# Optimization experiments

Hardware: AMD Instinct MI355X
Metric: run time of the kernel (lower is better)

The kernel has to match this reference:

```python
import jax, jax.numpy as jnp
import numpy as np

HIDDEN = 5120
N_HEADS = 16           # 128 total heads / DEVICE_NUM=8
Q_LORA = 1536
KV_LORA = 512
NOPE = 128
ROPE = 64
QK_DIM = NOPE + ROPE   # 192
V_DIM = 128
EPS = 1e-6
ROPE_BASE = 10000.0
SCALE_BY_DEVICE = 1.0 / 8.0
SOFTMAX_SCALE = QK_DIM ** -0.5
B, S = 1, 2048


def rms_norm(x, w, eps=EPS):
    v = jnp.mean(jnp.square(x), axis=-1, keepdims=True)
    return x * jax.lax.rsqrt(v + eps) * w


def rotate_half(x):
    h = x.shape[-1] // 2
    return jnp.concatenate([-x[..., h:], x[..., :h]], axis=-1)


def interleave(x):
    # DeepSeek rope layout: view(b,h,s,d//2,2).transpose(-1,-2).reshape(b,h,s,d)
    b, h, s, d = x.shape
    return jnp.swapaxes(x.reshape(b, h, s, d // 2, 2), -1, -2).reshape(b, h, s, d)


def setup_inputs() -> dict:
    key = jax.random.key(0)
    ks = jax.random.split(key, 8)
    w = 0.02
    hidden_states = jax.random.normal(ks[0], (B, S, HIDDEN), dtype=jnp.float32)
    position_ids = jnp.arange(S, dtype=jnp.int64 if jax.config.jax_enable_x64 else jnp.int32)[None, :]
    causal = jnp.tril(jnp.ones((S, S), dtype=bool))
    attention_mask = jnp.where(causal, 0.0, -1e9).astype(jnp.float32)[None, None]
    return {
        'hidden_states': hidden_states,
        'position_ids': position_ids,
        'attention_mask': attention_mask,
        'ln_w': jnp.ones((HIDDEN,), jnp.float32),
        'wq_a': jax.random.normal(ks[1], (Q_LORA, HIDDEN), jnp.float32) * w,
        'q_a_ln_w': jnp.ones((Q_LORA,), jnp.float32),
        'wq_b': jax.random.normal(ks[2], (N_HEADS * QK_DIM, Q_LORA), jnp.float32) * w,
        'wkv_a': jax.random.normal(ks[3], (KV_LORA + ROPE, HIDDEN), jnp.float32) * w,
        'kv_a_ln_w': jnp.ones((KV_LORA,), jnp.float32),
        'wkv_b': jax.random.normal(ks[4], (N_HEADS * (NOPE + V_DIM), KV_LORA), jnp.float32) * w,
        'wo': jax.random.normal(ks[5], (HIDDEN, N_HEADS * V_DIM), jnp.float32) * w,
    }


def reference(hidden_states, position_ids, attention_mask, ln_w, wq_a, q_a_ln_w,
              wq_b, wkv_a, kv_a_ln_w, wkv_b, wo):
    b, s, _ = hidden_states.shape
    residual = hidden_states * SCALE_BY_DEVICE
    h = rms_norm(hidden_states, ln_w)

    # Q low-rank decompression: q_a_proj -> RMSNorm -> q_b_proj
    q = rms_norm(h @ wq_a.T, q_a_ln_w) @ wq_b.T
    q = q.reshape(b, s, N_HEADS, QK_DIM).transpose(0, 2, 1, 3)  # b,h,s,192
    q_nope, q_pe = q[..., :NOPE], q[..., NOPE:]

    # KV low-rank: kv_a_proj_with_mqa -> split -> RMSNorm -> kv_b_proj
    ckv = h @ wkv_a.T                                           # b,s,512+64
    c_kv, k_pe = ckv[..., :KV_LORA], ckv[..., KV_LORA:]
    k_pe = k_pe[:, None, :, :]                                  # b,1,s,64
    kv = rms_norm(c_kv, kv_a_ln_w) @ wkv_b.T
    kv = kv.reshape(b, s, N_HEADS, NOPE + V_DIM).transpose(0, 2, 1, 3)
    k_nope, v = kv[..., :NOPE], kv[..., NOPE:]

    # RoPE (DeepSeek interleaved layout)
    inv_freq = 1.0 / (ROPE_BASE ** (jnp.arange(0, ROPE, 2, dtype=jnp.float32) / ROPE))
    freqs = position_ids.astype(jnp.float32)[..., None] * inv_freq  # b,s,32
    emb = jnp.concatenate([freqs, freqs], axis=-1)                  # b,s,64
    cos = jnp.cos(emb)[:, None]                                     # b,1,s,64
    sin = jnp.sin(emb)[:, None]
    q_pe = interleave(q_pe)
    k_pe = interleave(k_pe)
    q_pe = q_pe * cos + rotate_half(q_pe) * sin
    k_pe = k_pe * cos + rotate_half(k_pe) * sin

    k = jnp.concatenate([k_nope, jnp.broadcast_to(k_pe, (b, N_HEADS, s, ROPE))], axis=-1)
    qf = jnp.concatenate([q_nope, q_pe], axis=-1)

    scores = jnp.einsum('bhqd,bhkd->bhqk', qf, k) * SOFTMAX_SCALE + attention_mask
    attn = jax.nn.softmax(scores.astype(jnp.float32), axis=-1).astype(qf.dtype)
    out = jnp.einsum('bhqk,bhkd->bhqd', attn, v)                    # b,h,s,128
    out = out.transpose(0, 2, 1, 3).reshape(b, s, N_HEADS * V_DIM) @ wo.T

    hidden_states = residual + out
    return (hidden_states.astype(jnp.float32), k.astype(jnp.float32), v.astype(jnp.float32))
```

## Files before the change

kernel.cpp:

```cpp
#include <hip/hip_runtime.h>
#include <hip/hip_bf16.h>

typedef __hip_bfloat16 bf16;
typedef __attribute__((ext_vector_type(8))) short bf16x8;
typedef __attribute__((ext_vector_type(4))) float f32x4;

#define S_LEN   2048
#define HIDDEN  5120
#define NHEADS  16
#define QLORA   1536
#define KVLORA  512
#define QKD     192
#define VD      128
#define QN      (NHEADS*QKD)
#define KVN     (NHEADS*(128+VD))
#define QCKN    2112
#define SM_SCALE 0.07216878364870322f

__device__ __forceinline__ f32x4 mfma16(bf16x8 a, bf16x8 b, f32x4 c) {
  return __builtin_amdgcn_mfma_f32_16x16x32_bf16(a, b, c, 0, 0, 0);
}
__device__ __forceinline__ void g2l16(const void* g, void* l) {
  __builtin_amdgcn_global_load_lds((const __attribute__((address_space(1))) void*)g,
                                   (__attribute__((address_space(3))) void*)l, 16, 0, 0);
}
__device__ __forceinline__ bf16x8 ld8(const bf16* p) { return *(const bf16x8*)p; }

__global__ void init_k(float4* __restrict__ qa_ckv, int n_qa,
                       float4* __restrict__ q_f, int n_q)
{
  int i = blockIdx.x * 256 + threadIdx.x;
  if (i < n_qa) { qa_ckv[i] = (float4){0.f, 0.f, 0.f, 0.f}; return; }
  if ((i -= n_qa) < n_q) q_f[i] = (float4){0.f, 0.f, 0.f, 0.f};
}

__global__ void cvt_multi(const float* s0, bf16* d0, int n0,
                          const float* s1, bf16* d1, int n1,
                          const float* s2, bf16* d2, int n2,
                          const float* s3, bf16* d3, int n3,
                          const float* s4, bf16* d4, int n4s)
{
  int i = blockIdx.x * 256 + threadIdx.x;
  const float* s; bf16* d;
  if (i < n0) { s = s0; d = d0; }
  else if ((i -= n0) < n1) { s = s1; d = d1; }
  else if ((i -= n1) < n2) { s = s2; d = d2; }
  else if ((i -= n2) < n3) { s = s3; d = d3; }
  else if ((i -= n3) < n4s) { s = s4; d = d4; }
  else return;
  const float4 v = ((const float4*)s)[i];
  union { bf16 b[4]; unsigned long long u; } pk;
  pk.b[0] = __float2bfloat16(v.x);
  pk.b[1] = __float2bfloat16(v.y);
  pk.b[2] = __float2bfloat16(v.z);
  pk.b[3] = __float2bfloat16(v.w);
  *(unsigned long long*)(d + (size_t)i * 4) = pk.u;
}

__global__ void rmsnorm_k(const float* __restrict__ in, int istride, int C,
                          const float* __restrict__ w,
                          bf16* __restrict__ out, int ostride)
{
  const int row = blockIdx.x;
  const float* x = in + (size_t)row * istride;
  float ss = 0.f;
  for (int c = threadIdx.x; c < C; c += 256) { float v = x[c]; ss += v * v; }
  #pragma unroll
  for (int m = 32; m >= 1; m >>= 1) ss += __shfl_xor(ss, m, 64);
  __shared__ float red[4];
  if ((threadIdx.x & 63) == 0) red[threadIdx.x >> 6] = ss;
  __syncthreads();
  ss = red[0] + red[1] + red[2] + red[3];
  const float sc = rsqrtf(ss / (float)C + 1e-6f);
  bf16* o = out + (size_t)row * ostride;
  for (int c = threadIdx.x; c < C; c += 256)
    o[c] = __float2bfloat16(x[c] * sc * w[c]);
}

__global__ void rmsnorm2_k(const float* __restrict__ qackv,
                           const float* __restrict__ wq, const float* __restrict__ wk,
                           bf16* __restrict__ qa_n, bf16* __restrict__ ckv_n)
{
  const int r = blockIdx.x;
  const bool is_q = r < S_LEN;
  const int row = is_q ? r : r - S_LEN;
  const int C = is_q ? QLORA : KVLORA;
  const float* x = qackv + (size_t)row * QCKN + (is_q ? 0 : QLORA);
  const float* w = is_q ? wq : wk;
  bf16* o = (is_q ? qa_n + (size_t)row * QLORA : ckv_n + (size_t)row * KVLORA);
  float ss = 0.f;
  for (int c = threadIdx.x; c < C; c += 256) { float v = x[c]; ss += v * v; }
  #pragma unroll
  for (int m = 32; m >= 1; m >>= 1) ss += __shfl_xor(ss, m, 64);
  __shared__ float red[4];
  if ((threadIdx.x & 63) == 0) red[threadIdx.x >> 6] = ss;
  __syncthreads();
  ss = red[0] + red[1] + red[2] + red[3];
  const float sc = rsqrtf(ss / (float)C + 1e-6f);
  for (int c = threadIdx.x; c < C; c += 256)
    o[c] = __float2bfloat16(x[c] * sc * w[c]);
}

template<bool RESID, bool CLAMPN, bool ATOMIC>
__global__ __launch_bounds__(256, 4)
void gemm_nt(const bf16* __restrict__ A, const bf16* __restrict__ Bt,
             float* __restrict__ C, int M, int N, int lda, int klen,
             const float* __restrict__ resid, float rscale)
{
  __shared__ bf16 As[2 * 128 * 32];
  __shared__ bf16 Bs[2 * 128 * 32];
  const int tid = threadIdx.x;
  const int wave = tid >> 6;
  const int lane = tid & 63;
  const int l15 = lane & 15, quad = lane >> 4;
  const int bm = blockIdx.x * 128, bn = blockIdx.y * 128;
  const int kbase = blockIdx.z * klen;
  const int wm = (wave >> 1) * 64, wn = (wave & 1) * 64;

  const int srow = tid >> 2;
  const int scol = (tid & 3) * 8;
  const bf16* Ag0 = A + (size_t)(bm + srow) * lda + kbase + scol;
  const bf16* Ag1 = A + (size_t)(bm + 64 + srow) * lda + kbase + scol;
  int bn0 = bn + srow, bn1 = bn + 64 + srow;
  if (CLAMPN) { bn0 = min(bn0, N - 1); bn1 = min(bn1, N - 1); }
  const bf16* Bg0 = Bt + (size_t)bn0 * lda + kbase + scol;
  const bf16* Bg1 = Bt + (size_t)bn1 * lda + kbase + scol;

  char* AsW = (char*)As + wave * 1024;
  char* BsW = (char*)Bs + wave * 1024;

  f32x4 acc[4][4];
  #pragma unroll
  for (int i = 0; i < 4; i++)
    #pragma unroll
    for (int j = 0; j < 4; j++) acc[i][j] = (f32x4){0.f, 0.f, 0.f, 0.f};

  const int nk = klen >> 6;
  for (int kt = 0; kt < nk; ++kt) {
    const int k0 = kt << 6;
    #pragma unroll
    for (int c = 0; c < 2; ++c) {
      g2l16(Ag0 + k0 + c * 32, AsW + c * 8192);
      g2l16(Ag1 + k0 + c * 32, AsW + c * 8192 + 4096);
      g2l16(Bg0 + k0 + c * 32, BsW + c * 8192);
      g2l16(Bg1 + k0 + c * 32, BsW + c * 8192 + 4096);
    }
    __syncthreads();
    #pragma unroll
    for (int c = 0; c < 2; ++c) {
      bf16x8 af[4], bfr[4];
      #pragma unroll
      for (int i = 0; i < 4; i++)
        af[i] = ld8(As + c * 4096 + (wm + i * 16 + l15) * 32 + quad * 8);
      #pragma unroll
      for (int j = 0; j < 4; j++)
        bfr[j] = ld8(Bs + c * 4096 + (wn + j * 16 + l15) * 32 + quad * 8);
      #pragma unroll
      for (int i = 0; i < 4; i++)
        #pragma unroll
        for (int j = 0; j < 4; j++)
          acc[i][j] = mfma16(af[i], bfr[j], acc[i][j]);
    }
    __syncthreads();
  }

  #pragma unroll
  for (int i = 0; i < 4; i++)
    #pragma unroll
    for (int j = 0; j < 4; j++) {
      const int row = bm + wm + i * 16 + quad * 4;
      const int col = bn + wn + j * 16 + l15;
      if (!CLAMPN || col < N) {
        #pragma unroll
        for (int r = 0; r < 4; r++) {
          float v = acc[i][j][r];
          const size_t idx = (size_t)(row + r) * N + col;
          if (RESID) v += resid[idx] * rscale;
          if (ATOMIC) unsafeAtomicAdd(&C[idx], v);
          else        C[idx] = v;
        }
      }
    }
}

__global__ void rope_assemble_k(
    const float* __restrict__ q,
    const float* __restrict__ qackv,
    const float* __restrict__ kv,
    const int*   __restrict__ pos,
    float* __restrict__ k_out,
    bf16*  __restrict__ q_bf,
    bf16*  __restrict__ k_bf)
{
  const int s = blockIdx.x;
  const int t = threadIdx.x;
  __shared__ float cs[32], sn[32], kpe[64];
  const float p = (float)pos[s];
  if (t < 32) {
    const float inv = powf(10000.0f, -((float)(2 * t)) / 64.0f);
    const float f = p * inv;
    float si, c;
    sincosf(f, &si, &c);
    cs[t] = c; sn[t] = si;
    const float r0v = qackv[(size_t)s * QCKN + 2048 + 2 * t];
    const float r1v = qackv[(size_t)s * QCKN + 2048 + 2 * t + 1];
    kpe[t]      = r0v * c - r1v * si;
    kpe[32 + t] = r1v * c + r0v * si;
  }
  __syncthreads();
  for (int i = t; i < NHEADS * 128; i += 256) {
    const int h = i >> 7, d = i & 127;
    const size_t o = ((size_t)h * S_LEN + s) * QKD + d;
    const float kn = kv[(size_t)s * KVN + h * 256 + d];
    k_out[o] = kn;
    k_bf[o] = __float2bfloat16(kn);
    q_bf[o] = __float2bfloat16(q[(size_t)s * QN + h * QKD + d]);
  }
  for (int i = t; i < NHEADS * 32; i += 256) {
    const int h = i >> 5, jj = i & 31;
    const float r0v = q[(size_t)s * QN + h * QKD + 128 + 2 * jj];
    const float r1v = q[(size_t)s * QN + h * QKD + 128 + 2 * jj + 1];
    const float c = cs[jj], si = sn[jj];
    const size_t o = ((size_t)h * S_LEN + s) * QKD + 128;
    q_bf[o + jj]      = __float2bfloat16(r0v * c - r1v * si);
    q_bf[o + 32 + jj] = __float2bfloat16(r1v * c + r0v * si);
  }
  for (int i = t; i < NHEADS * 64; i += 256) {
    const int h = i >> 6, jj = i & 63;
    const float v = kpe[jj];
    const size_t o = ((size_t)h * S_LEN + s) * QKD + 128 + jj;
    k_out[o] = v;
    k_bf[o] = __float2bfloat16(v);
  }
}

__global__ void v_transpose_k(const float* __restrict__ kv,
                              float* __restrict__ v_out,
                              bf16* __restrict__ vt_bf)
{
  const int h = blockIdx.x, st = blockIdx.y, dt = blockIdx.z;
  __shared__ float tile[32][33];
  const int tx = threadIdx.x & 31;
  const int ty = (threadIdx.x >> 5) * 4;
  const int s0 = st * 32, d0 = dt * 32;
  #pragma unroll
  for (int r = 0; r < 4; r++) {
    const int sl = ty + r;
    const float v = kv[(size_t)(s0 + sl) * KVN + h * 256 + 128 + d0 + tx];
    v_out[((size_t)h * S_LEN + s0 + sl) * VD + d0 + tx] = v;
    tile[sl][tx] = v;
  }
  __syncthreads();
  #pragma unroll
  for (int r = 0; r < 4; r++) {
    const int dl = ty + r;
    vt_bf[((size_t)h * VD + d0 + dl) * S_LEN + s0 + tx] = __float2bfloat16(tile[tx][dl]);
  }
}

__global__ __launch_bounds__(256, 3)
void attn_k(const bf16* __restrict__ qb, const bf16* __restrict__ kb,
            const bf16* __restrict__ vt, bf16* __restrict__ aout)
{
  const int head = blockIdx.y;
  const int qt = (head < 8) ? blockIdx.x : (gridDim.x - 1 - blockIdx.x);
  const int wave = threadIdx.x >> 6, lane = threadIdx.x & 63;
  const int l15 = lane & 15, quad = lane >> 4;
  const int r0 = qt * 64 + wave * 16;

  const bf16* qh = qb + (size_t)head * S_LEN * QKD;
  const bf16* kh = kb + (size_t)head * S_LEN * QKD;
  const bf16* vh = vt + (size_t)head * VD * S_LEN;

  __shared__ bf16 Ks[6 * 64 * 32];
  __shared__ bf16 Vs[128 * 72];
  __shared__ bf16 Plds[4][16][72];

  const int tid = threadIdx.x;
  const int srow = wave * 16 + (lane >> 2);
  const int scol = (lane & 3) * 8;
  const bf16* ksrc = kh + (size_t)srow * QKD + scol;
  bf16* kdst = Ks + srow * 32 + scol;
  const int vrow = tid >> 1;
  const int vcol = (tid & 1) * 32;
  const bf16* vsrc = vh + (size_t)vrow * S_LEN + vcol;
  bf16* vdst = Vs + vrow * 72 + vcol;

  bf16x8 qf[6];
  #pragma unroll
  for (int c = 0; c < 6; ++c)
    qf[c] = ld8(qh + (size_t)(r0 + l15) * QKD + c * 32 + quad * 8);

  f32x4 O[8];
  #pragma unroll
  for (int d = 0; d < 8; ++d) O[d] = (f32x4){0.f, 0.f, 0.f, 0.f};
  float mrow[4] = {-1e30f, -1e30f, -1e30f, -1e30f};
  float lrow[4] = {0.f, 0.f, 0.f, 0.f};

  bf16x8 kreg[6], vreg[4];
  #pragma unroll
  for (int c = 0; c < 6; ++c) kreg[c] = ld8(ksrc + c * 32);
  #pragma unroll
  for (int c = 0; c < 4; ++c) vreg[c] = ld8(vsrc + c * 8);

  for (int j = 0; j <= qt; ++j) {
    __syncthreads();
    #pragma unroll
    for (int c = 0; c < 6; ++c) *(bf16x8*)(kdst + c * 2048) = kreg[c];
    #pragma unroll
    for (int c = 0; c < 4; ++c) *(bf16x8*)(vdst + c * 8) = vreg[c];
    __syncthreads();
    if (j < qt) {
      const bf16* src = ksrc + (size_t)(j + 1) * 64 * QKD;
      #pragma unroll
      for (int c = 0; c < 6; ++c) kreg[c] = ld8(src + c * 32);
      const bf16* vs2 = vsrc + (size_t)(j + 1) * 64;
      #pragma unroll
      for (int c = 0; c < 4; ++c) vreg[c] = ld8(vs2 + c * 8);
    }
    const int kc = j * 64;

    f32x4 S[4];
    #pragma unroll
    for (int nt = 0; nt < 4; ++nt) S[nt] = (f32x4){0.f, 0.f, 0.f, 0.f};
    #pragma unroll
    for (int c = 0; c < 6; ++c) {
      #pragma unroll
      for (int nt = 0; nt < 4; ++nt) {
        const bf16x8 kf = ld8(Ks + c * 2048 + (nt * 16 + l15) * 32 + quad * 8);
        S[nt] = mfma16(qf[c], kf, S[nt]);
      }
    }

    float mnew[4] = {-1e30f, -1e30f, -1e30f, -1e30f};
    if (j == qt) {
      #pragma unroll
      for (int nt = 0; nt < 4; ++nt) {
        const int col = kc + nt * 16 + l15;
        #pragma unroll
        for (int r = 0; r < 4; r++) {
          const int row = r0 + quad * 4 + r;
          const float v = (col <= row) ? S[nt][r] * SM_SCALE : -1e30f;
          S[nt][r] = v;
          mnew[r] = fmaxf(mnew[r], v);
        }
      }
    } else {
      #pragma unroll
      for (int nt = 0; nt < 4; ++nt)
        #pragma unroll
        for (int r = 0; r < 4; r++) {
          const float v = S[nt][r] * SM_SCALE;
          S[nt][r] = v;
          mnew[r] = fmaxf(mnew[r], v);
        }
    }
    #pragma unroll
    for (int m = 8; m >= 1; m >>= 1)
      #pragma unroll
      for (int r = 0; r < 4; r++)
        mnew[r] = fmaxf(mnew[r], __shfl_xor(mnew[r], m, 64));
    float alpha[4], ladd[4] = {0.f, 0.f, 0.f, 0.f};
    #pragma unroll
    for (int r = 0; r < 4; r++) {
      const float mi = fmaxf(mrow[r], mnew[r]);
      alpha[r] = __expf(mrow[r] - mi);
      mrow[r] = mi;
    }
    #pragma unroll
    for (int nt = 0; nt < 4; ++nt)
      #pragma unroll
      for (int r = 0; r < 4; r++) {
        const float pv = __expf(S[nt][r] - mrow[r]);
        S[nt][r] = pv;
        ladd[r] += pv;
      }
    #pragma unroll
    for (int m = 8; m >= 1; m >>= 1)
      #pragma unroll
      for (int r = 0; r < 4; r++) ladd[r] += __shfl_xor(ladd[r], m, 64);
    #pragma unroll
    for (int r = 0; r < 4; r++) lrow[r] = lrow[r] * alpha[r] + ladd[r];
    #pragma unroll
    for (int d = 0; d < 8; ++d)
      #pragma unroll
      for (int r = 0; r < 4; r++) O[d][r] *= alpha[r];

    #pragma unroll
    for (int nt = 0; nt < 4; ++nt)
      #pragma unroll
      for (int r = 0; r < 4; r++)
        Plds[wave][quad * 4 + r][nt * 16 + l15] = __float2bfloat16(S[nt][r]);

    #pragma unroll
    for (int kt = 0; kt < 2; ++kt) {
      const bf16x8 pf = ld8(&Plds[wave][l15][kt * 32 + quad * 8]);
      #pragma unroll
      for (int dt = 0; dt < 8; ++dt) {
        const bf16x8 vf = ld8(Vs + (dt * 16 + l15) * 72 + kt * 32 + quad * 8);
        O[dt] = mfma16(pf, vf, O[dt]);
      }
    }
  }

  #pragma unroll
  for (int dt = 0; dt < 8; ++dt) {
    const int col = head * VD + dt * 16 + l15;
    #pragma unroll
    for (int r = 0; r < 4; r++) {
      const int row = r0 + quad * 4 + r;
      aout[(size_t)row * (NHEADS * VD) + col] = __float2bfloat16(O[dt][r] / lrow[r]);
    }
  }
}

extern "C" void kernel_launch(void* const* d_in, const int* in_sizes, int n_in,
                              void* d_out, int out_size, void* d_ws, size_t ws_size,
                              hipStream_t stream)
{
  const float* hs      = (const float*)d_in[0];
  const int*   pos     = (const int*)  d_in[1];
  const float* ln_w    = (const float*)d_in[3];
  const float* wq_a    = (const float*)d_in[4];
  const float* q_a_ln  = (const float*)d_in[5];
  const float* wq_b    = (const float*)d_in[6];
  const float* wkv_a   = (const float*)d_in[7];
  const float* kv_a_ln = (const float*)d_in[8];
  const float* wkv_b   = (const float*)d_in[9];
  const float* wo      = (const float*)d_in[10];

  float* out_hidden = (float*)d_out;
  float* out_k = out_hidden + (size_t)S_LEN * HIDDEN;
  float* out_v = out_k + (size_t)NHEADS * S_LEN * QKD;

  char* ws = (char*)d_ws;
  size_t off = 0;
  auto alloc = [&](size_t bytes) { char* p = ws + off; off += (bytes + 255) & ~255ULL; return p; };

  bf16* h_b     = (bf16*)alloc((size_t)S_LEN * HIDDEN * 2);
  bf16* w1_b    = (bf16*)alloc((size_t)QCKN * HIDDEN * 2);
  bf16* wqb_b   = (bf16*)alloc((size_t)QN * QLORA * 2);
  bf16* wkvb_b  = (bf16*)alloc((size_t)KVN * KVLORA * 2);
  bf16* wo_b    = (bf16*)alloc((size_t)HIDDEN * (NHEADS * VD) * 2);
  float* qa_ckv = (float*)alloc((size_t)S_LEN * QCKN * 4);
  float* q_f    = (float*)alloc((size_t)S_LEN * QN * 4);
  bf16* qa_n    = (bf16*)alloc((size_t)S_LEN * QLORA * 2);
  bf16* ckv_n   = (bf16*)alloc((size_t)S_LEN * KVLORA * 2);
  float* kv_f   = (float*)alloc((size_t)S_LEN * KVN * 4);
  bf16* q_bf    = (bf16*)alloc((size_t)NHEADS * S_LEN * QKD * 2);
  bf16* k_bf    = (bf16*)alloc((size_t)NHEADS * S_LEN * QKD * 2);
  bf16* vt_bf   = (bf16*)alloc((size_t)NHEADS * VD * S_LEN * 2);
  bf16* attn_b  = (bf16*)alloc((size_t)S_LEN * (NHEADS * VD) * 2);

  {
    const int n_qa = (int)((size_t)S_LEN * QCKN / 4);
    const int n_q  = (int)((size_t)S_LEN * QN / 4);
    const int tot = n_qa + n_q;
    init_k<<<(tot + 255) / 256, 256, 0, stream>>>(
        (float4*)qa_ckv, n_qa, (float4*)q_f, n_q);
  }

  {
    const int n0 = (QLORA * HIDDEN) / 4;
    const int n1 = ((QCKN - QLORA) * HIDDEN) / 4;
    const int n2 = (QN * QLORA) / 4;
    const int n3 = (KVN * KVLORA) / 4;
    const int n4s = (HIDDEN * NHEADS * VD) / 4;
    const int tot = n0 + n1 + n2 + n3 + n4s;
    cvt_multi<<<(tot + 255) / 256, 256, 0, stream>>>(
        wq_a, w1_b, n0,
        wkv_a, w1_b + (size_t)QLORA * HIDDEN, n1,
        wq_b, wqb_b, n2,
        wkv_b, wkvb_b, n3,
        wo, wo_b, n4s);
  }

  rmsnorm_k<<<S_LEN, 256, 0, stream>>>(hs, HIDDEN, HIDDEN, ln_w, h_b, HIDDEN);

  gemm_nt<false, true, true><<<dim3(16, 17, 4), 256, 0, stream>>>(
      h_b, w1_b, qa_ckv, S_LEN, QCKN, HIDDEN, HIDDEN / 4, nullptr, 0.f);

  rmsnorm2_k<<<2 * S_LEN, 256, 0, stream>>>(qa_ckv, q_a_ln, kv_a_ln, qa_n, ckv_n);

  gemm_nt<false, false, true><<<dim3(16, QN / 128, 2), 256, 0, stream>>>(
      qa_n, wqb_b, q_f, S_LEN, QN, QLORA, QLORA / 2, nullptr, 0.f);
  gemm_nt<false, false, false><<<dim3(16, KVN / 128, 1), 256, 0, stream>>>(
      ckv_n, wkvb_b, kv_f, S_LEN, KVN, KVLORA, KVLORA, nullptr, 0.f);

  rope_assemble_k<<<S_LEN, 256, 0, stream>>>(q_f, qa_ckv, kv_f, pos, out_k, q_bf, k_bf);
  v_transpose_k<<<dim3(NHEADS, S_LEN / 32, VD / 32), 256, 0, stream>>>(kv_f, out_v, vt_bf);

  attn_k<<<dim3(S_LEN / 64, NHEADS), 256, 0, stream>>>(q_bf, k_bf, vt_bf, attn_b);

  gemm_nt<true, false, false><<<dim3(16, HIDDEN / 128, 1), 256, 0, stream>>>(
      attn_b, wo_b, out_hidden, S_LEN, HIDDEN, NHEADS * VD, NHEADS * VD, hs, 0.125f);

  (void)in_sizes; (void)n_in; (void)out_size; (void)ws_size;
}
```

Measured before the change: 595.6 us.

## Replace GEMMs with 256x256 swizzled-LDS ping-pong MFMA kernel and merge launches

Replaces the 128x128 gemm_nt with a 512-thread, 256x256-tile GEMM. It double-buffers XOR-swizzled LDS, interleaves its loads with MFMA phases using explicit barriers, vmcnt waits and setprio, and remaps blocks in an XCD-aware order. The first projection's N is padded to 2304 with zeroed weight rows so no clamping is needed. The q_b and kv_b GEMMs share one launch, and the attention output buffer reuses h_b. The aim is more data reuse per tile and fewer launches, at the cost of padding work, fewer blocks for the wo GEMM, and more complex synchronisation.

```diff
diff --git a/kernel.cpp b/kernel.cpp
--- a/kernel.cpp
+++ b/kernel.cpp
@@ -15,6 +15,7 @@
 #define QN      (NHEADS*QKD)
 #define KVN     (NHEADS*(128+VD))
 #define QCKN    2112
+#define QCKP    2304
 #define SM_SCALE 0.07216878364870322f
 
 __device__ __forceinline__ f32x4 mfma16(bf16x8 a, bf16x8 b, f32x4 c) {
@@ -26,12 +27,22 @@
 }
 __device__ __forceinline__ bf16x8 ld8(const bf16* p) { return *(const bf16x8*)p; }
 
-__global__ void init_k(float4* __restrict__ qa_ckv, int n_qa,
-                       float4* __restrict__ q_f, int n_q)
+__device__ __forceinline__ void bar() {
+  __builtin_amdgcn_sched_barrier(0);
+  __builtin_amdgcn_s_barrier();
+  __builtin_amdgcn_sched_barrier(0);
+}
+#define VMCNT(n) asm volatile("s_waitcnt vmcnt(" #n ")" ::: "memory")
+
+__global__ void init_k(float4* __restrict__ qa_ckv, int n0,
+                       float4* __restrict__ q_f, int n1,
+                       float4* __restrict__ w1pad, int n2)
 {
   int i = blockIdx.x * 256 + threadIdx.x;
-  if (i < n_qa) { qa_ckv[i] = (float4){0.f, 0.f, 0.f, 0.f}; return; }
-  if ((i -= n_qa) < n_q) q_f[i] = (float4){0.f, 0.f, 0.f, 0.f};
+  const float4 z = (float4){0.f, 0.f, 0.f, 0.f};
+  if (i < n0) { qa_ckv[i] = z; return; }
+  if ((i -= n0) < n1) { q_f[i] = z; return; }
+  if ((i -= n1) < n2) w1pad[i] = z;
 }
 
 __global__ void cvt_multi(const float* s0, bf16* d0, int n0,
@@ -85,7 +96,7 @@
   const bool is_q = r < S_LEN;
   const int row = is_q ? r : r - S_LEN;
   const int C = is_q ? QLORA : KVLORA;
-  const float* x = qackv + (size_t)row * QCKN + (is_q ? 0 : QLORA);
+  const float* x = qackv + (size_t)row * QCKP + (is_q ? 0 : QLORA);
   const float* w = is_q ? wq : wk;
   bf16* o = (is_q ? qa_n + (size_t)row * QLORA : ckv_n + (size_t)row * KVLORA);
   float ss = 0.f;
@@ -101,84 +112,143 @@
     o[c] = __float2bfloat16(x[c] * sc * w[c]);
 }
 
-template<bool RESID, bool CLAMPN, bool ATOMIC>
-__global__ __launch_bounds__(256, 4)
-void gemm_nt(const bf16* __restrict__ A, const bf16* __restrict__ Bt,
-             float* __restrict__ C, int M, int N, int lda, int klen,
-             const float* __restrict__ resid, float rscale)
-{
-  __shared__ bf16 As[2 * 128 * 32];
-  __shared__ bf16 Bs[2 * 128 * 32];
+struct GP {
+  const bf16* A; const bf16* Bt; float* C;
+  const float* resid;
+  float rscale;
+  int lda;
+  int NT;
+  int klen;
+  int N;
+  int flags;
+};
+
+#define LDA8(m, ks) ld8((const bf16*)(ldsw + s + wa_off + (((m) * 2048 + fx0) ^ ((ks) * 64))))
+#define LDB8(n, ks) ld8((const bf16*)(ldsw + s + 32768 + wb_off + (((n) * 2048 + fx0) ^ ((ks) * 64))))
+
+#define PH(M0, N0)                                                            \
+  do {                                                                        \
+    __builtin_amdgcn_s_setprio(1);                                            \
+    _Pragma("unroll") for (int mm = 0; mm < 4; ++mm)                          \
+      _Pragma("unroll") for (int nn = 0; nn < 2; ++nn) {                      \
+        acc[(M0)+mm][(N0)+nn] =                                               \
+            mfma16(af[0][(M0)+mm], bq[0][(N0)+nn], acc[(M0)+mm][(N0)+nn]);    \
+        acc[(M0)+mm][(N0)+nn] =                                               \
+            mfma16(af[1][(M0)+mm], bq[1][(N0)+nn], acc[(M0)+mm][(N0)+nn]);    \
+      }                                                                       \
+    __builtin_amdgcn_s_setprio(0);                                            \
+  } while (0)
+
+__global__ __launch_bounds__(512, 2)
+void gemm8p(GP p0, GP p1, int nb0, int q8)
+{
+  __shared__ char lds[131072];
+  const int orig = blockIdx.x;
+  int wg = (orig & 7) * q8 + (orig >> 3);
+  GP p = p0;
+  if (wg >= nb0) { p = p1; wg -= nb0; }
+  const int per = p.NT << 3;
+  const int zi = wg / per;
+  const int tb = wg - zi * per;
+  const int bm = (tb & 7) << 8;
+  const int bn = (tb >> 3) << 8;
+  const int lda = p.lda;
+  const int nt = p.klen >> 6;
+  const int kb = zi * p.klen;
+
   const int tid = threadIdx.x;
-  const int wave = tid >> 6;
   const int lane = tid & 63;
   const int l15 = lane & 15, quad = lane >> 4;
-  const int bm = blockIdx.x * 128, bn = blockIdx.y * 128;
-  const int kbase = blockIdx.z * klen;
-  const int wm = (wave >> 1) * 64, wn = (wave & 1) * 64;
-
-  const int srow = tid >> 2;
-  const int scol = (tid & 3) * 8;
-  const bf16* Ag0 = A + (size_t)(bm + srow) * lda + kbase + scol;
-  const bf16* Ag1 = A + (size_t)(bm + 64 + srow) * lda + kbase + scol;
-  int bn0 = bn + srow, bn1 = bn + 64 + srow;
-  if (CLAMPN) { bn0 = min(bn0, N - 1); bn1 = min(bn1, N - 1); }
-  const bf16* Bg0 = Bt + (size_t)bn0 * lda + kbase + scol;
-  const bf16* Bg1 = Bt + (size_t)bn1 * lda + kbase + scol;
-
-  char* AsW = (char*)As + wave * 1024;
-  char* BsW = (char*)Bs + wave * 1024;
-
-  f32x4 acc[4][4];
-  #pragma unroll
-  for (int i = 0; i < 4; i++)
-    #pragma unroll
-    for (int j = 0; j < 4; j++) acc[i][j] = (f32x4){0.f, 0.f, 0.f, 0.f};
-
-  const int nk = klen >> 6;
-  for (int kt = 0; kt < nk; ++kt) {
-    const int k0 = kt << 6;
-    #pragma unroll
-    for (int c = 0; c < 2; ++c) {
-      g2l16(Ag0 + k0 + c * 32, AsW + c * 8192);
-      g2l16(Ag1 + k0 + c * 32, AsW + c * 8192 + 4096);
-      g2l16(Bg0 + k0 + c * 32, BsW + c * 8192);
-      g2l16(Bg1 + k0 + c * 32, BsW + c * 8192 + 4096);
-    }
-    __syncthreads();
-    #pragma unroll
-    for (int c = 0; c < 2; ++c) {
-      bf16x8 af[4], bfr[4];
-      #pragma unroll
-      for (int i = 0; i < 4; i++)
-        af[i] = ld8(As + c * 4096 + (wm + i * 16 + l15) * 32 + quad * 8);
-      #pragma unroll
-      for (int j = 0; j < 4; j++)
-        bfr[j] = ld8(Bs + c * 4096 + (wn + j * 16 + l15) * 32 + quad * 8);
-      #pragma unroll
-      for (int i = 0; i < 4; i++)
-        #pragma unroll
-        for (int j = 0; j < 4; j++)
-          acc[i][j] = mfma16(af[i], bfr[j], acc[i][j]);
-    }
-    __syncthreads();
-  }
-
-  #pragma unroll
-  for (int i = 0; i < 4; i++)
-    #pragma unroll
-    for (int j = 0; j < 4; j++) {
-      const int row = bm + wm + i * 16 + quad * 4;
-      const int col = bn + wn + j * 16 + l15;
-      if (!CLAMPN || col < N) {
-        #pragma unroll
-        for (int r = 0; r < 4; r++) {
-          float v = acc[i][j][r];
-          const size_t idx = (size_t)(row + r) * N + col;
-          if (RESID) v += resid[idx] * rscale;
-          if (ATOMIC) unsafeAtomicAdd(&C[idx], v);
-          else        C[idx] = v;
-        }
+  const int waveu = __builtin_amdgcn_readfirstlane(tid >> 6);
+  const int wa = waveu >> 2, wn4 = waveu & 3, wb = wn4 >> 1;
+  const int woff = waveu << 10;
+  const int wa_off = wa << 14;
+  const int wb_off = (wb << 14) + ((wn4 & 1) << 13);
+
+  const int rb = tid >> 3;
+  const int celem = (((tid & 7) << 4) ^ ((rb & 7) << 4)) >> 1;
+  const int fx0 = l15 * 128 + (((quad << 4) ^ ((l15 & 7) << 4)));
+
+  const bf16* a0 = p.A + (size_t)(bm + rb) * lda + kb + celem;
+  const bf16* a1 = a0 + (size_t)128 * lda;
+  const bf16* b0 = p.Bt + (size_t)(bn + rb) * lda + kb + celem;
+  const bf16* b1 = b0 + (size_t)128 * lda;
+  const size_t lda64 = (size_t)64 * lda;
+  char* ldsw = (char*)lds;
+
+  auto stA = [&](int t, int h) {
+    const int ts = t < nt ? t : nt - 1;
+    const bf16* sp = (h ? a1 : a0) + ts * 64;
+    char* d = ldsw + ((t & 1) << 16) + (h << 14) + woff;
+    g2l16(sp, d);
+    g2l16(sp + lda64, d + 8192);
+  };
+  auto stB = [&](int t, int h) {
+    const int ts = t < nt ? t : nt - 1;
+    const bf16* sp = (h ? b1 : b0) + ts * 64;
+    char* d = ldsw + ((t & 1) << 16) + 32768 + (h << 14) + woff;
+    g2l16(sp, d);
+    g2l16(sp + lda64, d + 8192);
+  };
+
+  f32x4 acc[8][4];
+  #pragma unroll
+  for (int m = 0; m < 8; ++m)
+    #pragma unroll
+    for (int n = 0; n < 4; ++n) acc[m][n] = (f32x4){0.f, 0.f, 0.f, 0.f};
+  bf16x8 af[2][8], bq[2][4];
+
+  stA(0, 0); stA(0, 1); stB(0, 0); stB(0, 1); stA(1, 0); stA(1, 1);
+  VMCNT(4);
+  bar();
+
+  for (int t = 0; t < nt; ++t) {
+    const int s = (t & 1) << 16;
+    stB(t + 1, 0);
+    #pragma unroll
+    for (int ks = 0; ks < 2; ++ks) {
+      #pragma unroll
+      for (int m = 0; m < 4; ++m) af[ks][m] = LDA8(m, ks);
+      #pragma unroll
+      for (int n = 0; n < 2; ++n) bq[ks][n] = LDB8(n, ks);
+    }
+    bar(); PH(0, 0); bar();
+    stB(t + 1, 1);
+    #pragma unroll
+    for (int ks = 0; ks < 2; ++ks)
+      #pragma unroll
+      for (int m = 4; m < 8; ++m) af[ks][m] = LDA8(m, ks);
+    bar(); PH(4, 0); bar();
+    stA(t + 2, 0);
+    #pragma unroll
+    for (int ks = 0; ks < 2; ++ks)
+      #pragma unroll
+      for (int n = 2; n < 4; ++n) bq[ks][n] = LDB8(n, ks);
+    bar(); PH(4, 2); bar();
+    stA(t + 2, 1);
+    bar(); PH(0, 2);
+    VMCNT(4);
+    bar();
+  }
+  VMCNT(0);
+
+  const int rowb = bm + wa * 128 + quad * 4;
+  const int colb = bn + wn4 * 64 + l15;
+  const bool at = (p.flags & 1) != 0;
+  const bool rs = (p.flags & 2) != 0;
+  #pragma unroll
+  for (int m = 0; m < 8; ++m)
+    #pragma unroll
+    for (int n = 0; n < 4; ++n) {
+      const int col = colb + n * 16;
+      #pragma unroll
+      for (int r = 0; r < 4; ++r) {
+        const int row = rowb + m * 16 + r;
+        float v = acc[m][n][r];
+        const size_t idx = (size_t)row * p.N + col;
+        if (rs) v += p.resid[idx] * p.rscale;
+        if (at) unsafeAtomicAdd(&p.C[idx], v);
+        else    p.C[idx] = v;
       }
     }
 }
@@ -202,8 +272,8 @@
     float si, c;
     sincosf(f, &si, &c);
     cs[t] = c; sn[t] = si;
-    const float r0v = qackv[(size_t)s * QCKN + 2048 + 2 * t];
-    const float r1v = qackv[(size_t)s * QCKN + 2048 + 2 * t + 1];
+    const float r0v = qackv[(size_t)s * QCKP + 2048 + 2 * t];
+    const float r1v = qackv[(size_t)s * QCKP + 2048 + 2 * t + 1];
     kpe[t]      = r0v * c - r1v * si;
     kpe[32 + t] = r1v * c + r0v * si;
   }
@@ -438,11 +508,11 @@
   auto alloc = [&](size_t bytes) { char* p = ws + off; off += (bytes + 255) & ~255ULL; return p; };
 
   bf16* h_b     = (bf16*)alloc((size_t)S_LEN * HIDDEN * 2);
-  bf16* w1_b    = (bf16*)alloc((size_t)QCKN * HIDDEN * 2);
+  bf16* w1_b    = (bf16*)alloc((size_t)QCKP * HIDDEN * 2);
   bf16* wqb_b   = (bf16*)alloc((size_t)QN * QLORA * 2);
   bf16* wkvb_b  = (bf16*)alloc((size_t)KVN * KVLORA * 2);
   bf16* wo_b    = (bf16*)alloc((size_t)HIDDEN * (NHEADS * VD) * 2);
-  float* qa_ckv = (float*)alloc((size_t)S_LEN * QCKN * 4);
+  float* qa_ckv = (float*)alloc((size_t)S_LEN * QCKP * 4);
   float* q_f    = (float*)alloc((size_t)S_LEN * QN * 4);
   bf16* qa_n    = (bf16*)alloc((size_t)S_LEN * QLORA * 2);
   bf16* ckv_n   = (bf16*)alloc((size_t)S_LEN * KVLORA * 2);
@@ -450,14 +520,16 @@
   bf16* q_bf    = (bf16*)alloc((size_t)NHEADS * S_LEN * QKD * 2);
   bf16* k_bf    = (bf16*)alloc((size_t)NHEADS * S_LEN * QKD * 2);
   bf16* vt_bf   = (bf16*)alloc((size_t)NHEADS * VD * S_LEN * 2);
-  bf16* attn_b  = (bf16*)alloc((size_t)S_LEN * (NHEADS * VD) * 2);
+  bf16* attn_b  = h_b;
 
   {
-    const int n_qa = (int)((size_t)S_LEN * QCKN / 4);
-    const int n_q  = (int)((size_t)S_LEN * QN / 4);
-    const int tot = n_qa + n_q;
+    const int n0 = (int)((size_t)S_LEN * QCKP / 4);
+    const int n1 = (int)((size_t)S_LEN * QN / 4);
+    const int n2 = (int)((size_t)(QCKP - QCKN) * HIDDEN * 2 / 16);
+    const int tot = n0 + n1 + n2;
     init_k<<<(tot + 255) / 256, 256, 0, stream>>>(
-        (float4*)qa_ckv, n_qa, (float4*)q_f, n_q);
+        (float4*)qa_ckv, n0, (float4*)q_f, n1,
+        (float4*)(w1_b + (size_t)QCKN * HIDDEN), n2);
   }
 
   {
@@ -477,23 +549,28 @@
 
   rmsnorm_k<<<S_LEN, 256, 0, stream>>>(hs, HIDDEN, HIDDEN, ln_w, h_b, HIDDEN);
 
-  gemm_nt<false, true, true><<<dim3(16, 17, 4), 256, 0, stream>>>(
-      h_b, w1_b, qa_ckv, S_LEN, QCKN, HIDDEN, HIDDEN / 4, nullptr, 0.f);
+  {
+    GP g1 = {h_b, w1_b, qa_ckv, nullptr, 0.f, HIDDEN, 9, 1024, QCKP, 1};
+    gemm8p<<<dim3(360), 512, 0, stream>>>(g1, g1, 360, 45);
+  }
 
   rmsnorm2_k<<<2 * S_LEN, 256, 0, stream>>>(qa_ckv, q_a_ln, kv_a_ln, qa_n, ckv_n);
 
-  gemm_nt<false, false, true><<<dim3(16, QN / 128, 2), 256, 0, stream>>>(
-      qa_n, wqb_b, q_f, S_LEN, QN, QLORA, QLORA / 2, nullptr, 0.f);
-  gemm_nt<false, false, false><<<dim3(16, KVN / 128, 1), 256, 0, stream>>>(
-      ckv_n, wkvb_b, kv_f, S_LEN, KVN, KVLORA, KVLORA, nullptr, 0.f);
+  {
+    GP g2 = {qa_n, wqb_b, q_f, nullptr, 0.f, QLORA, 12, 768, QN, 1};
+    GP g3 = {ckv_n, wkvb_b, kv_f, nullptr, 0.f, KVLORA, 16, 512, KVN, 0};
+    gemm8p<<<dim3(320), 512, 0, stream>>>(g2, g3, 192, 40);
+  }
 
   rope_assemble_k<<<S_LEN, 256, 0, stream>>>(q_f, qa_ckv, kv_f, pos, out_k, q_bf, k_bf);
   v_transpose_k<<<dim3(NHEADS, S_LEN / 32, VD / 32), 256, 0, stream>>>(kv_f, out_v, vt_bf);
 
   attn_k<<<dim3(S_LEN / 64, NHEADS), 256, 0, stream>>>(q_bf, k_bf, vt_bf, attn_b);
 
-  gemm_nt<true, false, false><<<dim3(16, HIDDEN / 128, 1), 256, 0, stream>>>(
-      attn_b, wo_b, out_hidden, S_LEN, HIDDEN, NHEADS * VD, NHEADS * VD, hs, 0.125f);
+  {
+    GP g4 = {attn_b, wo_b, out_hidden, hs, 0.125f, NHEADS * VD, 20, 2048, HIDDEN, 2};
+    gemm8p<<<dim3(160), 512, 0, stream>>>(g4, g4, 160, 20);
+  }
 
   (void)in_sizes; (void)n_in; (void)out_size; (void)ws_size;
 }
```

Result: slower. 651.5 us (+9.4%).

## Replace atomic split-K accumulation with partial buffers reduced in consumer kernels

Applied to the files above, without the earlier changes.

The split-K GEMMs for the q_a/kv_a and q_b projections now write each K-slice to its own partial buffer instead of doing atomic adds into a zero-initialised output. The RMSNorm and RoPE-assemble kernels sum the partials when they read them, and the k_pe slice is reduced into a small separate buffer. This removes the zero-init kernel and the atomic read-modify-write traffic. In exchange it writes and reads more partial data, and it reuses one workspace region for the partials, q_f and kv_f through aliasing.

```diff
diff --git a/kernel.cpp b/kernel.cpp
--- a/kernel.cpp
+++ b/kernel.cpp
@@ -25,14 +25,6 @@
                                    (__attribute__((address_space(3))) void*)l, 16, 0, 0);
 }
 __device__ __forceinline__ bf16x8 ld8(const bf16* p) { return *(const bf16x8*)p; }
-
-__global__ void init_k(float4* __restrict__ qa_ckv, int n_qa,
-                       float4* __restrict__ q_f, int n_q)
-{
-  int i = blockIdx.x * 256 + threadIdx.x;
-  if (i < n_qa) { qa_ckv[i] = (float4){0.f, 0.f, 0.f, 0.f}; return; }
-  if ((i -= n_qa) < n_q) q_f[i] = (float4){0.f, 0.f, 0.f, 0.f};
-}
 
 __global__ void cvt_multi(const float* s0, bf16* d0, int n0,
                           const float* s1, bf16* d1, int n1,
@@ -77,19 +69,26 @@
     o[c] = __float2bfloat16(x[c] * sc * w[c]);
 }
 
-__global__ void rmsnorm2_k(const float* __restrict__ qackv,
+__global__ void rmsnorm2_k(const float* __restrict__ parts,
                            const float* __restrict__ wq, const float* __restrict__ wk,
-                           bf16* __restrict__ qa_n, bf16* __restrict__ ckv_n)
+                           bf16* __restrict__ qa_n, bf16* __restrict__ ckv_n,
+                           float* __restrict__ kpe_sum)
 {
   const int r = blockIdx.x;
   const bool is_q = r < S_LEN;
   const int row = is_q ? r : r - S_LEN;
   const int C = is_q ? QLORA : KVLORA;
-  const float* x = qackv + (size_t)row * QCKN + (is_q ? 0 : QLORA);
+  const size_t PS = (size_t)S_LEN * QCKN;
+  const float* x0 = parts + (size_t)row * QCKN + (is_q ? 0 : QLORA);
   const float* w = is_q ? wq : wk;
   bf16* o = (is_q ? qa_n + (size_t)row * QLORA : ckv_n + (size_t)row * KVLORA);
+  __shared__ float xs[QLORA];
   float ss = 0.f;
-  for (int c = threadIdx.x; c < C; c += 256) { float v = x[c]; ss += v * v; }
+  for (int c = threadIdx.x; c < C; c += 256) {
+    const float v = x0[c] + x0[PS + c] + x0[2 * PS + c] + x0[3 * PS + c];
+    xs[c] = v;
+    ss += v * v;
+  }
   #pragma unroll
   for (int m = 32; m >= 1; m >>= 1) ss += __shfl_xor(ss, m, 64);
   __shared__ float red[4];
@@ -98,10 +97,15 @@
   ss = red[0] + red[1] + red[2] + red[3];
   const float sc = rsqrtf(ss / (float)C + 1e-6f);
   for (int c = threadIdx.x; c < C; c += 256)
-    o[c] = __float2bfloat16(x[c] * sc * w[c]);
-}
-
-template<bool RESID, bool CLAMPN, bool ATOMIC>
+    o[c] = __float2bfloat16(xs[c] * sc * w[c]);
+  if (!is_q) {
+    const float* kp = parts + (size_t)row * QCKN + 2048;
+    for (int c = threadIdx.x; c < 64; c += 256)
+      kpe_sum[row * 64 + c] = kp[c] + kp[PS + c] + kp[2 * PS + c] + kp[3 * PS + c];
+  }
+}
+
+template<bool RESID, bool CLAMPN, bool SPLIT>
 __global__ __launch_bounds__(256, 4)
 void gemm_nt(const bf16* __restrict__ A, const bf16* __restrict__ Bt,
              float* __restrict__ C, int M, int N, int lda, int klen,
@@ -164,6 +168,8 @@
     __syncthreads();
   }
 
+  float* Cb = C;
+  if (SPLIT) Cb += (size_t)blockIdx.z * ((size_t)S_LEN * (size_t)N);
   #pragma unroll
   for (int i = 0; i < 4; i++)
     #pragma unroll
@@ -176,16 +182,15 @@
           float v = acc[i][j][r];
           const size_t idx = (size_t)(row + r) * N + col;
           if (RESID) v += resid[idx] * rscale;
-          if (ATOMIC) unsafeAtomicAdd(&C[idx], v);
-          else        C[idx] = v;
+          Cb[idx] = v;
         }
       }
     }
 }
 
 __global__ void rope_assemble_k(
-    const float* __restrict__ q,
-    const float* __restrict__ qackv,
+    const float* __restrict__ qp,
+    const float* __restrict__ kpe_sum,
     const float* __restrict__ kv,
     const int*   __restrict__ pos,
     float* __restrict__ k_out,
@@ -194,6 +199,7 @@
 {
   const int s = blockIdx.x;
   const int t = threadIdx.x;
+  const size_t QPS = (size_t)S_LEN * QN;
   __shared__ float cs[32], sn[32], kpe[64];
   const float p = (float)pos[s];
   if (t < 32) {
@@ -202,8 +208,8 @@
     float si, c;
     sincosf(f, &si, &c);
     cs[t] = c; sn[t] = si;
-    const float r0v = qackv[(size_t)s * QCKN + 2048 + 2 * t];
-    const float r1v = qackv[(size_t)s * QCKN + 2048 + 2 * t + 1];
+    const float r0v = kpe_sum[(size_t)s * 64 + 2 * t];
+    const float r1v = kpe_sum[(size_t)s * 64 + 2 * t + 1];
     kpe[t]      = r0v * c - r1v * si;
     kpe[32 + t] = r1v * c + r0v * si;
   }
@@ -214,12 +220,14 @@
     const float kn = kv[(size_t)s * KVN + h * 256 + d];
     k_out[o] = kn;
     k_bf[o] = __float2bfloat16(kn);
-    q_bf[o] = __float2bfloat16(q[(size_t)s * QN + h * QKD + d]);
+    const size_t qi = (size_t)s * QN + h * QKD + d;
+    q_bf[o] = __float2bfloat16(qp[qi] + qp[QPS + qi]);
   }
   for (int i = t; i < NHEADS * 32; i += 256) {
     const int h = i >> 5, jj = i & 31;
-    const float r0v = q[(size_t)s * QN + h * QKD + 128 + 2 * jj];
-    const float r1v = q[(size_t)s * QN + h * QKD + 128 + 2 * jj + 1];
+    const size_t qi = (size_t)s * QN + h * QKD + 128 + 2 * jj;
+    const float r0v = qp[qi] + qp[QPS + qi];
+    const float r1v = qp[qi + 1] + qp[QPS + qi + 1];
     const float c = cs[jj], si = sn[jj];
     const size_t o = ((size_t)h * S_LEN + s) * QKD + 128;
     q_bf[o + jj]      = __float2bfloat16(r0v * c - r1v * si);
@@ -442,23 +450,17 @@
   bf16* wqb_b   = (bf16*)alloc((size_t)QN * QLORA * 2);
   bf16* wkvb_b  = (bf16*)alloc((size_t)KVN * KVLORA * 2);
   bf16* wo_b    = (bf16*)alloc((size_t)HIDDEN * (NHEADS * VD) * 2);
-  float* qa_ckv = (float*)alloc((size_t)S_LEN * QCKN * 4);
-  float* q_f    = (float*)alloc((size_t)S_LEN * QN * 4);
+  char* region  = alloc((size_t)2 * S_LEN * QN * 4 + (size_t)S_LEN * KVN * 4);
+  float* qa_parts = (float*)region;
+  float* q_f      = (float*)region;
+  float* kv_f     = (float*)(region + (size_t)2 * S_LEN * QN * 4);
+  float* kpe_sum = (float*)alloc((size_t)S_LEN * 64 * 4);
   bf16* qa_n    = (bf16*)alloc((size_t)S_LEN * QLORA * 2);
   bf16* ckv_n   = (bf16*)alloc((size_t)S_LEN * KVLORA * 2);
-  float* kv_f   = (float*)alloc((size_t)S_LEN * KVN * 4);
   bf16* q_bf    = (bf16*)alloc((size_t)NHEADS * S_LEN * QKD * 2);
   bf16* k_bf    = (bf16*)alloc((size_t)NHEADS * S_LEN * QKD * 2);
   bf16* vt_bf   = (bf16*)alloc((size_t)NHEADS * VD * S_LEN * 2);
   bf16* attn_b  = (bf16*)alloc((size_t)S_LEN * (NHEADS * VD) * 2);
-
-  {
-    const int n_qa = (int)((size_t)S_LEN * QCKN / 4);
-    const int n_q  = (int)((size_t)S_LEN * QN / 4);
-    const int tot = n_qa + n_q;
-    init_k<<<(tot + 255) / 256, 256, 0, stream>>>(
-        (float4*)qa_ckv, n_qa, (float4*)q_f, n_q);
-  }
 
   {
     const int n0 = (QLORA * HIDDEN) / 4;
@@ -478,16 +480,18 @@
   rmsnorm_k<<<S_LEN, 256, 0, stream>>>(hs, HIDDEN, HIDDEN, ln_w, h_b, HIDDEN);
 
   gemm_nt<false, true, true><<<dim3(16, 17, 4), 256, 0, stream>>>(
-      h_b, w1_b, qa_ckv, S_LEN, QCKN, HIDDEN, HIDDEN / 4, nullptr, 0.f);
-
-  rmsnorm2_k<<<2 * S_LEN, 256, 0, stream>>>(qa_ckv, q_a_ln, kv_a_ln, qa_n, ckv_n);
+      h_b, w1_b, qa_parts, S_LEN, QCKN, HIDDEN, HIDDEN / 4, nullptr, 0.f);
+
+  rmsnorm2_k<<<2 * S_LEN, 256, 0, stream>>>(qa_parts, q_a_ln, kv_a_ln,
+                                            qa_n, ckv_n, kpe_sum);
 
   gemm_nt<false, false, true><<<dim3(16, QN / 128, 2), 256, 0, stream>>>(
       qa_n, wqb_b, q_f, S_LEN, QN, QLORA, QLORA / 2, nullptr, 0.f);
   gemm_nt<false, false, false><<<dim3(16, KVN / 128, 1), 256, 0, stream>>>(
       ckv_n, wkvb_b, kv_f, S_LEN, KVN, KVLORA, KVLORA, nullptr, 0.f);
 
-  rope_assemble_k<<<S_LEN, 256, 0, stream>>>(q_f, qa_ckv, kv_f, pos, out_k, q_bf, k_bf);
+  rope_assemble_k<<<S_LEN, 256, 0, stream>>>(q_f, kpe_sum, kv_f, pos,
+                                             out_k, q_bf, k_bf);
   v_transpose_k<<<dim3(NHEADS, S_LEN / 32, VD / 32), 256, 0, stream>>>(kv_f, out_v, vt_bf);
 
   attn_k<<<dim3(S_LEN / 64, NHEADS), 256, 0, stream>>>(q_bf, k_bf, vt_bf, attn_b);
```

After: 539.3 us. 9.5% less time.
